# Kernel tuning notes

Measured on AMD Instinct MI355X. Metric: run time of the kernel, lower is better.

The kernel has to match this reference:

```python
import jax, jax.numpy as jnp
import numpy as np
import math

V, TB, C, H, L = 50257, 1024, 1024, 16, 8
B, T = 2, 1024
D = C // H


def setup_inputs() -> dict:
    key = jax.random.key(0)
    ks = jax.random.split(key, 16)
    s = 0.02
    n = lambda k, shp: (jax.random.normal(k, shp, jnp.float32) * s)
    inp = {
        "idx": jax.random.randint(ks[0], (B, T), 0, V),
        "tok_emb": n(ks[1], (V, C)),
        "pos_emb": n(ks[2], (1, TB, C)),
        # per-layer stacked params (torch Linear convention: W is [out, in])
        "Wq": n(ks[3], (L, C, C)), "bq": jnp.zeros((L, C)),
        "Wk": n(ks[4], (L, C, C)), "bk": jnp.zeros((L, C)),
        "Wv": n(ks[5], (L, C, C)), "bv": jnp.zeros((L, C)),
        "Wp": n(ks[6], (L, C, C)), "bp": jnp.zeros((L, C)),
        "ln1_w": jnp.ones((L, C)), "ln1_b": jnp.zeros((L, C)),
        "ln2_w": jnp.ones((L, C)), "ln2_b": jnp.zeros((L, C)),
        "W1": n(ks[7], (L, 4 * C, C)), "b1": jnp.zeros((L, 4 * C)),
        "W2": n(ks[8], (L, C, 4 * C)), "b2": jnp.zeros((L, C)),
        "lnf_w": jnp.ones((C,)), "lnf_b": jnp.zeros((C,)),
        "head_w": n(ks[9], (V, C)),
    }
    return inp


def _layer_norm(x, w, b, eps=1e-5):
    mu = x.mean(-1, keepdims=True)
    var = x.var(-1, keepdims=True)
    return (x - mu) * jax.lax.rsqrt(var + eps) * w + b


def _gpt_forward(idx, tok_emb, pos_emb, Wq, bq, Wk, bk, Wv, bv, Wp, bp,
                 ln1_w, ln1_b, ln2_w, ln2_b, W1, b1, W2, b2, lnf_w, lnf_b, head_w):
    b, t = idx.shape
    x = tok_emb[idx] + pos_emb[:, :t, :]  # [B, T, C]; drop = identity (eval)
    causal = jnp.tril(jnp.ones((t, t), dtype=bool))  # [T, T]
    scale = 1.0 / math.sqrt(D)

    def block(x, p):
        (wq, bq_, wk, bk_, wv, bv_, wp, bp_, l1w, l1b, l2w, l2b, w1, b1_, w2, b2_) = p
        h = _layer_norm(x, l1w, l1b)
        q = (h @ wq.T + bq_).reshape(b, t, H, D).transpose(0, 2, 1, 3)  # [B,H,T,D]
        k = (h @ wk.T + bk_).reshape(b, t, H, D).transpose(0, 2, 1, 3)
        v = (h @ wv.T + bv_).reshape(b, t, H, D).transpose(0, 2, 1, 3)
        att = jnp.einsum("bhqd,bhkd->bhqk", q, k) * scale
        att = jnp.where(causal, att, -jnp.inf)
        att = jax.nn.softmax(att, axis=-1)
        y = jnp.einsum("bhqk,bhkd->bhqd", att, v)
        y = y.transpose(0, 2, 1, 3).reshape(b, t, C)
        x = x + (y @ wp.T + bp_)
        h2 = _layer_norm(x, l2w, l2b)
        m = jax.nn.gelu(h2 @ w1.T + b1_, approximate=False)  # torch nn.GELU (erf)
        x = x + (m @ w2.T + b2_)
        return x, None

    params = (Wq, bq, Wk, bk, Wv, bv, Wp, bp, ln1_w, ln1_b, ln2_w, ln2_b, W1, b1, W2, b2)
    x, _ = jax.lax.scan(block, x, params)
    x = _layer_norm(x, lnf_w, lnf_b)
    logits = x @ head_w.T  # [B, T, V]
    return logits


def reference(idx, tok_emb, pos_emb, Wq, bq, Wk, bk, Wv, bv, Wp, bp,
              ln1_w, ln1_b, ln2_w, ln2_b, W1, b1, W2, b2, lnf_w, lnf_b, head_w):
    return _gpt_forward(idx, tok_emb, pos_emb, Wq, bq, Wk, bk, Wv, bv, Wp, bp,
                        ln1_w, ln1_b, ln2_w, ln2_b, W1, b1, W2, b2, lnf_w, lnf_b, head_w)
```

## Files before the change

### kernel.cpp

```cpp
#include <hip/hip_runtime.h>
#include <math.h>

#define V_ 50257
#define C_ 1024
#define H_ 16
#define L_ 8
#define B_ 2
#define T_ 1024
#define BT_ 2048
#define CC_ (C_*C_)
#define QLD_ 3072

typedef unsigned short ushort_t;
using bf16x8 = __attribute__((ext_vector_type(8))) short;
using f32x4  = __attribute__((ext_vector_type(4))) float;

__device__ __forceinline__ ushort_t f2bf(float f){
  union { float f; unsigned u; } a; a.f = f;
  unsigned r = a.u + 0x7fffu + ((a.u >> 16) & 1u);
  return (ushort_t)(r >> 16);
}

__device__ __forceinline__ float wave_sum(float v){
  #pragma unroll
  for(int o=32;o>0;o>>=1) v += __shfl_down(v,o,64);
  return v;
}

__global__ __launch_bounds__(256) void cvt_blk(const float* __restrict__ s, ushort_t* __restrict__ d,
    long inner4, int nblk, long dstStride4){
  long total = inner4 * nblk;
  for(long i = (long)blockIdx.x*256 + threadIdx.x; i < total; i += (long)gridDim.x*256){
    long blk = i / inner4, r = i - blk*inner4;
    float4 v = ((const float4*)s)[i];
    ushort4 o; o.x=f2bf(v.x); o.y=f2bf(v.y); o.z=f2bf(v.z); o.w=f2bf(v.w);
    ((ushort4*)d)[blk*dstStride4 + r] = o;
  }
}

__global__ __launch_bounds__(256) void pack_qkv_bias(const float* __restrict__ bq,
    const float* __restrict__ bk, const float* __restrict__ bv, float* __restrict__ dst){
  int i = blockIdx.x*256 + threadIdx.x;
  int l = i / QLD_, c = i - l*QLD_;
  float v;
  if(c < C_)            v = bq[l*C_ + c];
  else if(c < 2*C_)     v = bk[l*C_ + c - C_];
  else                  v = bv[l*C_ + c - 2*C_];
  dst[i] = v;
}

__global__ __launch_bounds__(256) void embed_kernel(const int* __restrict__ idx,
    const float* __restrict__ tok, const float* __restrict__ pos, float* __restrict__ x){
  int i = blockIdx.x*256 + threadIdx.x;
  int c = i & (C_-1); int bt = i >> 10; int t = bt & (T_-1);
  x[i] = tok[(size_t)idx[bt]*C_ + c] + pos[t*C_ + c];
}

__global__ __launch_bounds__(256) void ln_kernel(const float* in, const float* __restrict__ w,
    const float* __restrict__ b, float* outF, ushort_t* outB){
  int row = blockIdx.x;
  const float* xr = in + (size_t)row*C_;
  float vals[4]; float sum=0.f, sq=0.f;
  #pragma unroll
  for(int l=0;l<4;l++){ float v = xr[threadIdx.x + l*256]; vals[l]=v; sum+=v; sq+=v*v; }
  __shared__ float r1[4], r2[4];
  float s1 = wave_sum(sum), s2 = wave_sum(sq);
  int wid = threadIdx.x>>6, lane = threadIdx.x&63;
  if(lane==0){ r1[wid]=s1; r2[wid]=s2; }
  __syncthreads();
  float tot  = r1[0]+r1[1]+r1[2]+r1[3];
  float tot2 = r2[0]+r2[1]+r2[2]+r2[3];
  float mu  = tot * (1.f/C_);
  float var = tot2 * (1.f/C_) - mu*mu;
  float inv = rsqrtf(var + 1e-5f);
  #pragma unroll
  for(int l=0;l<4;l++){
    int c = threadIdx.x + l*256;
    float v = (vals[l]-mu)*inv*w[c] + b[c];
    if(outB) outB[(size_t)row*C_ + c] = f2bf(v);
    else     outF[(size_t)row*C_ + c] = v;
  }
}

template<int BN>
__global__ __launch_bounds__(256) void gemm_mfma(
    const ushort_t* __restrict__ A, const ushort_t* __restrict__ W,
    const float* __restrict__ bias, const float* resid,
    float* outF, ushort_t* outB,
    int M, int N, int K, int act, int nt)
{
  constexpr int BM = 128;
  constexpr int NSB = BN/16;
  constexpr int NBF = BN/32;
  __shared__ __align__(16) short sA[2][8*512];
  __shared__ __align__(16) short sB[2][NSB*512];
  const int tid  = threadIdx.x;
  const int lane = tid & 63, wid = tid >> 6;
  const int wr = wid >> 1, wc = wid & 1;
  const int nwg = gridDim.x * gridDim.y;
  const int lid = blockIdx.x + gridDim.x * blockIdx.y;
  const int swz = (lid & 7) * (nwg >> 3) + (lid >> 3);
  const int m0 = (swz % gridDim.x) * BM, n0 = (swz / gridDim.x) * BN;
  const int r16 = lane & 15, kq = lane >> 4;

  auto stage = [&](int buf, int k0){
    #pragma unroll
    for(int s2=0; s2<2; ++s2){
      int s = wid*2 + s2;
      const ushort_t* g = A + (size_t)(m0 + s*16 + r16)*K + k0 + kq*8;
      __builtin_amdgcn_global_load_lds((const __attribute__((address_space(1))) void*)g,
          (__attribute__((address_space(3))) void*)&sA[buf][s*512], 16, 0, 0);
    }
    #pragma unroll
    for(int s2=0; s2<NSB/4; ++s2){
      int s = wid*(NSB/4) + s2;
      int gn = n0 + s*16 + r16; if(gn >= N) gn = N-1;
      const ushort_t* g = W + (size_t)gn*K + k0 + kq*8;
      __builtin_amdgcn_global_load_lds((const __attribute__((address_space(1))) void*)g,
          (__attribute__((address_space(3))) void*)&sB[buf][s*512], 16, 0, 0);
    }
  };

  f32x4 acc[4][NBF];
  #pragma unroll
  for(int i=0;i<4;i++)
    #pragma unroll
    for(int j=0;j<NBF;j++) acc[i][j] = (f32x4){0.f,0.f,0.f,0.f};

  const int NT = K >> 5;
  stage(0, 0);
  int cur = 0;
  for(int t=0; t<NT; ++t){
    __syncthreads();
    if(t+1 < NT) stage(cur^1, (t+1)*32);
    bf16x8 af[4], bfr[NBF];
    #pragma unroll
    for(int m=0;m<4;m++) af[m] = *(const bf16x8*)&sA[cur][(wr*4+m)*512 + lane*8];
    #pragma unroll
    for(int n=0;n<NBF;n++) bfr[n] = *(const bf16x8*)&sB[cur][(wc*NBF+n)*512 + lane*8];
    #pragma unroll
    for(int m=0;m<4;m++)
      #pragma unroll
      for(int n=0;n<NBF;n++)
        acc[m][n] = __builtin_amdgcn_mfma_f32_16x16x32_bf16(af[m], bfr[n], acc[m][n], 0, 0, 0);
    cur ^= 1;
  }

  const int colb = n0 + wc*(BN/2);
  #pragma unroll
  for(int m=0;m<4;m++){
    int rowb = m0 + wr*64 + m*16 + kq*4;
    #pragma unroll
    for(int n=0;n<NBF;n++){
      int col = colb + n*16 + r16;
      if(col >= N) continue;
      float bv = bias ? bias[col] : 0.f;
      #pragma unroll
      for(int i=0;i<4;i++){
        int row = rowb + i;
        float v = acc[m][n][i] + bv;
        if(act) v = 0.5f*v*(1.f + erff(v*0.70710678118654752f));
        if(resid) v += resid[(size_t)row*N + col];
        if(outB) outB[(size_t)row*N + col] = f2bf(v);
        else if(nt) __builtin_nontemporal_store(v, &outF[(size_t)row*N + col]);
        else outF[(size_t)row*N + col] = v;
      }
    }
  }
}

__global__ __launch_bounds__(256) void flash_kernel(const ushort_t* __restrict__ qkv,
    ushort_t* __restrict__ y){
  const int tid = threadIdx.x, lane = tid & 63, wid = tid >> 6;
  const int r16 = lane & 15, kq = lane >> 4;
  const int lid = blockIdx.x + 16*blockIdx.y;
  const int swz = (lid & 7)*64 + (lid >> 3);
  const int qt = swz & 15, bh = swz >> 4;
  const int b = bh >> 4, h = bh & 15;
  const int q0 = qt*64, qw0 = q0 + wid*16;
  const int qa = qw0 + r16;

  __shared__ __align__(16) short Kt[8][512];
  __shared__ __align__(16) short VT[64][68];
  __shared__ __align__(16) short Pl[4][16][68];
  __shared__ __align__(16) short Ol[4][16][68];

  const size_t rowQ = (size_t)(b*T_ + qa)*QLD_ + h*64 + kq*8;
  bf16x8 qf0 = *(const bf16x8*)(qkv + rowQ);
  bf16x8 qf1 = *(const bf16x8*)(qkv + rowQ + 32);

  f32x4 acc[4];
  #pragma unroll
  for(int t=0;t<4;t++) acc[t] = (f32x4){0.f,0.f,0.f,0.f};
  float m_r = -INFINITY, l_r = 0.f;

  const int njt = qt + 1;
  for(int jt=0; jt<njt; ++jt){
    __syncthreads();
    #pragma unroll
    for(int s2=0;s2<2;s2++){
      int s = wid*2 + s2;
      const ushort_t* g = qkv + (size_t)(b*T_ + jt*64 + (s>>1)*16 + r16)*QLD_
                          + C_ + h*64 + (s&1)*32 + kq*8;
      __builtin_amdgcn_global_load_lds((const __attribute__((address_space(1))) void*)g,
          (__attribute__((address_space(3))) void*)&Kt[s][lane*8], 16, 0, 0);
    }
    #pragma unroll
    for(int a2=0;a2<2;a2++){
      int d0 = (a2*4 + wid)*8;
      bf16x8 vv = *(const bf16x8*)(qkv + (size_t)(b*T_ + jt*64 + lane)*QLD_ + 2*C_ + h*64 + d0);
      #pragma unroll
      for(int j=0;j<8;j++) VT[d0+j][lane] = vv[j];
    }
    __syncthreads();

    f32x4 st[4];
    __builtin_amdgcn_s_setprio(1);
    #pragma unroll
    for(int kr=0;kr<4;kr++){
      st[kr] = (f32x4){0.f,0.f,0.f,0.f};
      st[kr] = __builtin_amdgcn_mfma_f32_16x16x32_bf16(*(const bf16x8*)&Kt[kr*2+0][lane*8], qf0, st[kr], 0,0,0);
      st[kr] = __builtin_amdgcn_mfma_f32_16x16x32_bf16(*(const bf16x8*)&Kt[kr*2+1][lane*8], qf1, st[kr], 0,0,0);
    }
    __builtin_amdgcn_s_setprio(0);

    float vals[16]; float mx = m_r;
    if(jt == njt-1){
      #pragma unroll
      for(int kr=0;kr<4;kr++)
        #pragma unroll
        for(int i=0;i<4;i++){
          int ka = jt*64 + kr*16 + 4*kq + i;
          float v = (ka <= qa) ? st[kr][i]*0.125f : -INFINITY;
          vals[kr*4+i] = v; mx = fmaxf(mx, v);
        }
    } else {
      #pragma unroll
      for(int kr=0;kr<4;kr++)
        #pragma unroll
        for(int i=0;i<4;i++){
          float v = st[kr][i]*0.125f;
          vals[kr*4+i] = v; mx = fmaxf(mx, v);
        }
    }
    mx = fmaxf(mx, __shfl_xor(mx, 16, 64));
    mx = fmaxf(mx, __shfl_xor(mx, 32, 64));
    float alpha = __expf(m_r - mx);
    float ps = 0.f;
    #pragma unroll
    for(int kr=0;kr<4;kr++){
      float p0 = __expf(vals[kr*4+0]-mx), p1 = __expf(vals[kr*4+1]-mx);
      float p2 = __expf(vals[kr*4+2]-mx), p3 = __expf(vals[kr*4+3]-mx);
      ps += (p0+p1)+(p2+p3);
      unsigned u0 = (unsigned)f2bf(p0) | ((unsigned)f2bf(p1)<<16);
      unsigned u1 = (unsigned)f2bf(p2) | ((unsigned)f2bf(p3)<<16);
      *(unsigned*)&Pl[wid][r16][kr*16 + 4*kq]     = u0;
      *(unsigned*)&Pl[wid][r16][kr*16 + 4*kq + 2] = u1;
    }
    ps += __shfl_xor(ps, 16, 64);
    ps += __shfl_xor(ps, 32, 64);
    l_r = l_r*alpha + ps; m_r = mx;
    #pragma unroll
    for(int t=0;t<4;t++)
      #pragma unroll
      for(int j=0;j<4;j++) acc[t][j] *= alpha;

    union { bf16x8 v8; uint2 u2[2]; } pf, vf;
    __builtin_amdgcn_s_setprio(1);
    #pragma unroll
    for(int ks2=0; ks2<2; ks2++){
      pf.u2[0] = *(const uint2*)&Pl[wid][r16][ks2*32 + kq*8];
      pf.u2[1] = *(const uint2*)&Pl[wid][r16][ks2*32 + kq*8 + 4];
      #pragma unroll
      for(int db=0; db<4; db++){
        vf.u2[0] = *(const uint2*)&VT[16*db + r16][ks2*32 + kq*8];
        vf.u2[1] = *(const uint2*)&VT[16*db + r16][ks2*32 + kq*8 + 4];
        acc[db] = __builtin_amdgcn_mfma_f32_16x16x32_bf16(vf.v8, pf.v8, acc[db], 0,0,0);
      }
    }
    __builtin_amdgcn_s_setprio(0);
  }

  float linv = 1.f / l_r;
  #pragma unroll
  for(int db=0; db<4; db++)
    #pragma unroll
    for(int i=0;i<4;i++)
      Ol[wid][r16][16*db + 4*kq + i] = (short)f2bf(acc[db][i]*linv);
  int q = lane >> 2, c0 = (lane & 3)*16;
  const short* src = &Ol[wid][q][c0];
  uint2 a0 = *(const uint2*)(src+0), a1 = *(const uint2*)(src+4);
  uint2 a2 = *(const uint2*)(src+8), a3 = *(const uint2*)(src+12);
  ushort_t* dst = y + (size_t)(b*T_ + qw0 + q)*C_ + h*64 + c0;
  uint4 w0 = {a0.x, a0.y, a1.x, a1.y}, w1 = {a2.x, a2.y, a3.x, a3.y};
  *(uint4*)(dst+0) = w0;
  *(uint4*)(dst+8) = w1;
}

__global__ __launch_bounds__(256) void gemm_nt(const float* __restrict__ A, const float* __restrict__ W,
    const float* __restrict__ bias, const float* resid, float* Cm,
    int M, int N, int K, int act){
  __shared__ float As[16][68];
  __shared__ float Bs[16][68];
  int m0 = blockIdx.y*64, n0 = blockIdx.x*64;
  int tid = threadIdx.x;
  int tx = tid & 15, ty = tid >> 4;
  float acc[4][4] = {};
  for(int k0=0;k0<K;k0+=16){
    #pragma unroll
    for(int l=0;l<4;l++){
      int li = tid + l*256;
      int r = li >> 4, c = li & 15;
      int gm = m0 + r, gn = n0 + r, gk = k0 + c;
      As[c][r] = (gm<M) ? A[(size_t)gm*K + gk] : 0.f;
      Bs[c][r] = (gn<N) ? W[(size_t)gn*K + gk] : 0.f;
    }
    __syncthreads();
    #pragma unroll
    for(int k=0;k<16;k++){
      float4 av = *(const float4*)&As[k][ty*4];
      float4 bv = *(const float4*)&Bs[k][tx*4];
      float a[4] = {av.x, av.y, av.z, av.w};
      float b4[4] = {bv.x, bv.y, bv.z, bv.w};
      #pragma unroll
      for(int i=0;i<4;i++)
        #pragma unroll
        for(int j=0;j<4;j++)
          acc[i][j] = fmaf(a[i], b4[j], acc[i][j]);
    }
    __syncthreads();
  }
  #pragma unroll
  for(int i=0;i<4;i++){
    int m = m0 + ty*4 + i; if(m>=M) continue;
    #pragma unroll
    for(int j=0;j<4;j++){
      int n = n0 + tx*4 + j; if(n>=N) continue;
      float v = acc[i][j];
      if(bias) v += bias[n];
      if(act)  v = 0.5f*v*(1.f + erff(v*0.70710678118654752f));
      if(resid) v += resid[(size_t)m*N + n];
      Cm[(size_t)m*N + n] = v;
    }
  }
}

extern "C" void kernel_launch(void* const* d_in, const int* in_sizes, int n_in,
                              void* d_out, int out_size, void* d_ws, size_t ws_size,
                              hipStream_t stream) {
  const int*   idx  = (const int*)  d_in[0];
  const float* tok  = (const float*)d_in[1];
  const float* pos  = (const float*)d_in[2];
  const float* Wq   = (const float*)d_in[3];
  const float* bq   = (const float*)d_in[4];
  const float* Wk   = (const float*)d_in[5];
  const float* bk   = (const float*)d_in[6];
  const float* Wv   = (const float*)d_in[7];
  const float* bv   = (const float*)d_in[8];
  const float* Wp   = (const float*)d_in[9];
  const float* bp   = (const float*)d_in[10];
  const float* ln1w = (const float*)d_in[11];
  const float* ln1b = (const float*)d_in[12];
  const float* ln2w = (const float*)d_in[13];
  const float* ln2b = (const float*)d_in[14];
  const float* W1   = (const float*)d_in[15];
  const float* b1   = (const float*)d_in[16];
  const float* W2   = (const float*)d_in[17];
  const float* b2   = (const float*)d_in[18];
  const float* lnfw = (const float*)d_in[19];
  const float* lnfb = (const float*)d_in[20];
  const float* headw= (const float*)d_in[21];

  float* out = (float*)d_out;
  ushort_t* qkvb = (ushort_t*)(out);
  ushort_t* hb   = (ushort_t*)(out + 3145728);
  ushort_t* yb   = (ushort_t*)(out + 4194304);
  ushort_t* mb   = (ushort_t*)(out + 5242880);
  ushort_t* wqkv = (ushort_t*)(out + 9437184);
  ushort_t* wpb  = (ushort_t*)(out + 22020096);
  ushort_t* w1b  = (ushort_t*)(out + 26214400);
  ushort_t* w2b  = (ushort_t*)(out + 42991616);
  float*    bqkv = out + 59768832;
  float*    x    = (float*)d_ws;
  ushort_t* xb   = (ushort_t*)((float*)d_ws + 2097152);
  ushort_t* whb  = (ushort_t*)((float*)d_ws + 3145728);
  const bool big = ws_size >= (size_t)28877312 * 4;

  cvt_blk<<<2048,256,0,stream>>>(Wq, wqkv,          CC_/4, L_, 3*CC_/4);
  cvt_blk<<<2048,256,0,stream>>>(Wk, wqkv + CC_,    CC_/4, L_, 3*CC_/4);
  cvt_blk<<<2048,256,0,stream>>>(Wv, wqkv + 2*CC_,  CC_/4, L_, 3*CC_/4);
  cvt_blk<<<2048,256,0,stream>>>(Wp, wpb,  (long)L_*CC_/4,   1, (long)L_*CC_/4);
  cvt_blk<<<2048,256,0,stream>>>(W1, w1b,  (long)L_*CC_,     1, (long)L_*CC_);
  cvt_blk<<<2048,256,0,stream>>>(W2, w2b,  (long)L_*CC_,     1, (long)L_*CC_);
  if(big) cvt_blk<<<2048,256,0,stream>>>(headw, whb, (long)V_*C_/4, 1, (long)V_*C_/4);
  pack_qkv_bias<<<L_*QLD_/256,256,0,stream>>>(bq, bk, bv, bqkv);

  embed_kernel<<<BT_*C_/256, 256, 0, stream>>>(idx, tok, pos, x);

  for(int l=0;l<L_;l++){
    ln_kernel<<<BT_,256,0,stream>>>(x, ln1w + l*C_, ln1b + l*C_, nullptr, hb);
    gemm_mfma<128><<<dim3(BT_/128, QLD_/128),256,0,stream>>>(hb, wqkv + (size_t)l*3*CC_,
        bqkv + l*QLD_, nullptr, nullptr, qkvb, BT_, QLD_, C_, 0, 0);
    flash_kernel<<<dim3(T_/64, B_*H_),256,0,stream>>>(qkvb, yb);
    gemm_mfma<64><<<dim3(BT_/128, C_/64),256,0,stream>>>(yb, wpb + (size_t)l*CC_,
        bp + l*C_, x, x, nullptr, BT_, C_, C_, 0, 0);
    ln_kernel<<<BT_,256,0,stream>>>(x, ln2w + l*C_, ln2b + l*C_, nullptr, hb);
    gemm_mfma<128><<<dim3(BT_/128, 4*C_/128),256,0,stream>>>(hb, w1b + (size_t)l*4*CC_,
        b1 + (size_t)l*4*C_, nullptr, nullptr, mb, BT_, 4*C_, C_, 1, 0);
    gemm_mfma<64><<<dim3(BT_/128, C_/64),256,0,stream>>>(mb, w2b + (size_t)l*4*CC_,
        b2 + l*C_, x, x, nullptr, BT_, C_, 4*C_, 0, 0);
  }

  if(big){
    ln_kernel<<<BT_,256,0,stream>>>(x, lnfw, lnfb, nullptr, xb);
    gemm_mfma<128><<<dim3(BT_/128, (V_+127)/128),256,0,stream>>>(xb, whb,
        nullptr, nullptr, out, nullptr, BT_, V_, C_, 0, 1);
  } else {
    ln_kernel<<<BT_,256,0,stream>>>(x, lnfw, lnfb, x, nullptr);
    gemm_nt<<<dim3((V_+63)/64, BT_/64),256,0,stream>>>(x, headw, nullptr, nullptr, out,
                                                       BT_, V_, C_, 0);
  }
}
```

Measured before the change: 2.870 ms.

## Add 256x256 eight-wave pipelined GEMM for the LM head

Adds a new 512-thread GEMM kernel with 256x256 output tiles, K-steps of 64 and a four-phase schedule. In each phase it issues async global-to-LDS loads for a future half-tile while the waves run MFMAs on the current quadrant, gated by explicit vmcnt waits and raw barriers. It replaces the 128x128 gemm_mfma for the vocabulary projection, the largest GEMM, to raise data reuse and overlap loads with compute. In exchange it uses more LDS and registers, and the hand-placed waitcnt and barrier ordering is fragile. The remaining edits only introduce address-space macros.

```diff
diff --git a/kernel.cpp b/kernel.cpp
--- a/kernel.cpp
+++ b/kernel.cpp
@@ -14,6 +14,12 @@
 typedef unsigned short ushort_t;
 using bf16x8 = __attribute__((ext_vector_type(8))) short;
 using f32x4  = __attribute__((ext_vector_type(4))) float;
+
+#define AS1 __attribute__((address_space(1)))
+#define AS3 __attribute__((address_space(3)))
+#define VMCNT6() asm volatile("s_waitcnt vmcnt(6)" ::: "memory")
+#define VMCNT0() asm volatile("s_waitcnt vmcnt(0)" ::: "memory")
+#define RBAR()   asm volatile("s_barrier" ::: "memory")
 
 __device__ __forceinline__ ushort_t f2bf(float f){
   union { float f; unsigned u; } a; a.f = f;
@@ -108,16 +114,16 @@
     for(int s2=0; s2<2; ++s2){
       int s = wid*2 + s2;
       const ushort_t* g = A + (size_t)(m0 + s*16 + r16)*K + k0 + kq*8;
-      __builtin_amdgcn_global_load_lds((const __attribute__((address_space(1))) void*)g,
-          (__attribute__((address_space(3))) void*)&sA[buf][s*512], 16, 0, 0);
+      __builtin_amdgcn_global_load_lds((const AS1 void*)g,
+          (AS3 void*)&sA[buf][s*512], 16, 0, 0);
     }
     #pragma unroll
     for(int s2=0; s2<NSB/4; ++s2){
       int s = wid*(NSB/4) + s2;
       int gn = n0 + s*16 + r16; if(gn >= N) gn = N-1;
       const ushort_t* g = W + (size_t)gn*K + k0 + kq*8;
-      __builtin_amdgcn_global_load_lds((const __attribute__((address_space(1))) void*)g,
-          (__attribute__((address_space(3))) void*)&sB[buf][s*512], 16, 0, 0);
+      __builtin_amdgcn_global_load_lds((const AS1 void*)g,
+          (AS3 void*)&sB[buf][s*512], 16, 0, 0);
     }
   };
 
@@ -167,6 +173,151 @@
       }
     }
   }
+}
+
+__global__ __launch_bounds__(512) void gemm_8ph(
+    const ushort_t* __restrict__ A, const ushort_t* __restrict__ W,
+    float* __restrict__ outF, int M, int N, int K, int gx)
+{
+  __shared__ __align__(16) short sA[2][2][8192];
+  __shared__ __align__(16) short sB[2][2][8192];
+  const int tid = threadIdx.x, lane = tid & 63;
+  const int wid = tid >> 6, wm = wid & 1, wn = wid >> 1;
+  const int r16 = lane & 15, kq = lane >> 4;
+  const int nwg = gridDim.x;
+  const int L = blockIdx.x;
+  const int swz = (L & 7) * (nwg >> 3) + (L >> 3);
+  const int m0 = (swz % gx) * 256, n0 = (swz / gx) * 256;
+
+  auto stage = [&](int buf, int half, int isB, int k0){
+    const ushort_t* base = isB ? W : A;
+    const int off0 = (isB ? n0 : m0) + half*128;
+    short* dst0 = isB ? &sB[buf][half][0] : &sA[buf][half][0];
+    #pragma unroll
+    for(int i=0;i<2;i++){
+      int sub = i*4 + (tid>>7);
+      int rem = tid & 127;
+      int row = off0 + sub*16 + (rem & 15);
+      if(isB && row >= N) row = N-1;
+      int kk = k0 + ((rem>>6)&1)*32 + ((rem>>4)&3)*8;
+      __builtin_amdgcn_global_load_lds((const AS1 void*)(base + (size_t)row*K + kk),
+          (AS3 void*)(dst0 + i*4096 + tid*8), 16, 0, 0);
+    }
+  };
+
+  f32x4 acc[2][2][4][2];
+  #pragma unroll
+  for(int a=0;a<2;a++)
+    #pragma unroll
+    for(int b=0;b<2;b++)
+      #pragma unroll
+      for(int m=0;m<4;m++)
+        #pragma unroll
+        for(int n=0;n<2;n++) acc[a][b][m][n] = (f32x4){0.f,0.f,0.f,0.f};
+
+  const int NT = K >> 6;
+  stage(0,0,0, 0); stage(0,0,1, 0); stage(0,1,1, 0); stage(0,1,0, 0);
+  if(NT>1){ stage(1,0,0, 64); stage(1,0,1, 64); stage(1,1,1, 64); }
+  VMCNT6();
+  RBAR();
+
+  bf16x8 af[4][2], bfr[2][2][2];
+
+  for(int t=0; t<NT; ++t){
+    const int buf = t & 1;
+    const int k1 = (t+1)<<6, k2 = (t+2)<<6;
+    const bool s1 = (t+1) < NT, s2 = (t+2) < NT;
+
+    if(s1) stage(buf^1, 1, 0, k1);
+    #pragma unroll
+    for(int m=0;m<4;m++)
+      #pragma unroll
+      for(int ks=0;ks<2;ks++)
+        af[m][ks] = *(const bf16x8*)&sA[buf][0][(wm*4+m)*1024 + ks*512 + lane*8];
+    #pragma unroll
+    for(int n=0;n<2;n++)
+      #pragma unroll
+      for(int ks=0;ks<2;ks++)
+        bfr[0][n][ks] = *(const bf16x8*)&sB[buf][0][(wn*2+n)*1024 + ks*512 + lane*8];
+    RBAR();
+    __builtin_amdgcn_s_setprio(1);
+    #pragma unroll
+    for(int m=0;m<4;m++)
+      #pragma unroll
+      for(int n=0;n<2;n++)
+        #pragma unroll
+        for(int ks=0;ks<2;ks++)
+          acc[0][0][m][n] = __builtin_amdgcn_mfma_f32_16x16x32_bf16(af[m][ks], bfr[0][n][ks], acc[0][0][m][n], 0,0,0);
+    __builtin_amdgcn_s_setprio(0);
+    RBAR();
+
+    if(s2) stage(buf, 0, 0, k2);
+    #pragma unroll
+    for(int n=0;n<2;n++)
+      #pragma unroll
+      for(int ks=0;ks<2;ks++)
+        bfr[1][n][ks] = *(const bf16x8*)&sB[buf][1][(wn*2+n)*1024 + ks*512 + lane*8];
+    RBAR();
+    __builtin_amdgcn_s_setprio(1);
+    #pragma unroll
+    for(int m=0;m<4;m++)
+      #pragma unroll
+      for(int n=0;n<2;n++)
+        #pragma unroll
+        for(int ks=0;ks<2;ks++)
+          acc[0][1][m][n] = __builtin_amdgcn_mfma_f32_16x16x32_bf16(af[m][ks], bfr[1][n][ks], acc[0][1][m][n], 0,0,0);
+    __builtin_amdgcn_s_setprio(0);
+    RBAR();
+
+    if(s2) stage(buf, 0, 1, k2);
+    #pragma unroll
+    for(int m=0;m<4;m++)
+      #pragma unroll
+      for(int ks=0;ks<2;ks++)
+        af[m][ks] = *(const bf16x8*)&sA[buf][1][(wm*4+m)*1024 + ks*512 + lane*8];
+    RBAR();
+    __builtin_amdgcn_s_setprio(1);
+    #pragma unroll
+    for(int m=0;m<4;m++)
+      #pragma unroll
+      for(int n=0;n<2;n++)
+        #pragma unroll
+        for(int ks=0;ks<2;ks++)
+          acc[1][1][m][n] = __builtin_amdgcn_mfma_f32_16x16x32_bf16(af[m][ks], bfr[1][n][ks], acc[1][1][m][n], 0,0,0);
+    __builtin_amdgcn_s_setprio(0);
+    RBAR();
+
+    if(s2) stage(buf, 1, 1, k2);
+    if(s2) { VMCNT6(); } else { VMCNT0(); }
+    RBAR();
+    __builtin_amdgcn_s_setprio(1);
+    #pragma unroll
+    for(int m=0;m<4;m++)
+      #pragma unroll
+      for(int n=0;n<2;n++)
+        #pragma unroll
+        for(int ks=0;ks<2;ks++)
+          acc[1][0][m][n] = __builtin_amdgcn_mfma_f32_16x16x32_bf16(af[m][ks], bfr[0][n][ks], acc[1][0][m][n], 0,0,0);
+    __builtin_amdgcn_s_setprio(0);
+    RBAR();
+  }
+
+  #pragma unroll
+  for(int mh=0;mh<2;mh++)
+    #pragma unroll
+    for(int nh=0;nh<2;nh++)
+      #pragma unroll
+      for(int m=0;m<4;m++){
+        int rowb = m0 + mh*128 + wm*64 + m*16 + kq*4;
+        #pragma unroll
+        for(int n=0;n<2;n++){
+          int col = n0 + nh*128 + wn*32 + n*16 + r16;
+          if(col >= N) continue;
+          #pragma unroll
+          for(int i=0;i<4;i++)
+            __builtin_nontemporal_store(acc[mh][nh][m][n][i], &outF[(size_t)(rowb+i)*N + col]);
+        }
+      }
 }
 
 __global__ __launch_bounds__(256) void flash_kernel(const ushort_t* __restrict__ qkv,
@@ -202,8 +353,8 @@
       int s = wid*2 + s2;
       const ushort_t* g = qkv + (size_t)(b*T_ + jt*64 + (s>>1)*16 + r16)*QLD_
                           + C_ + h*64 + (s&1)*32 + kq*8;
-      __builtin_amdgcn_global_load_lds((const __attribute__((address_space(1))) void*)g,
-          (__attribute__((address_space(3))) void*)&Kt[s][lane*8], 16, 0, 0);
+      __builtin_amdgcn_global_load_lds((const AS1 void*)g,
+          (AS3 void*)&Kt[s][lane*8], 16, 0, 0);
     }
     #pragma unroll
     for(int a2=0;a2<2;a2++){
@@ -413,8 +564,8 @@
 
   if(big){
     ln_kernel<<<BT_,256,0,stream>>>(x, lnfw, lnfb, nullptr, xb);
-    gemm_mfma<128><<<dim3(BT_/128, (V_+127)/128),256,0,stream>>>(xb, whb,
-        nullptr, nullptr, out, nullptr, BT_, V_, C_, 0, 1);
+    gemm_8ph<<<dim3((BT_/256) * ((V_+255)/256)),512,0,stream>>>(xb, whb, out,
+        BT_, V_, C_, BT_/256);
   } else {
     ln_kernel<<<BT_,256,0,stream>>>(x, lnfw, lnfb, x, nullptr);
     gemm_nt<<<dim3((V_+63)/64, BT_/64),256,0,stream>>>(x, headw, nullptr, nullptr, out,
```

Result: no change. 2.867 ms (-0.1%).

## Double-buffer K and V tiles in flash attention to overlap loads with compute

Applied to the files above, without the earlier changes.

The flash attention kernel now keeps two LDS buffers for K and transposed V. The next tile's K (async global-to-LDS) and V (into registers) are prefetched while the current tile's QK and PV MFMAs run, then V is written to the alternate buffer at the end of the iteration. This cuts the loop to one barrier per tile and hides global load latency, at the cost of doubled LDS for K/V, extra live registers, and possible lower occupancy. The GEMM change is a macro cleanup only.

```diff
diff --git a/kernel.cpp b/kernel.cpp
--- a/kernel.cpp
+++ b/kernel.cpp
@@ -14,6 +14,10 @@
 typedef unsigned short ushort_t;
 using bf16x8 = __attribute__((ext_vector_type(8))) short;
 using f32x4  = __attribute__((ext_vector_type(4))) float;
+
+#define AS1 __attribute__((address_space(1)))
+#define AS3 __attribute__((address_space(3)))
+#define VMCNT0() asm volatile("s_waitcnt vmcnt(0)" ::: "memory")
 
 __device__ __forceinline__ ushort_t f2bf(float f){
   union { float f; unsigned u; } a; a.f = f;
@@ -108,16 +112,16 @@
     for(int s2=0; s2<2; ++s2){
       int s = wid*2 + s2;
       const ushort_t* g = A + (size_t)(m0 + s*16 + r16)*K + k0 + kq*8;
-      __builtin_amdgcn_global_load_lds((const __attribute__((address_space(1))) void*)g,
-          (__attribute__((address_space(3))) void*)&sA[buf][s*512], 16, 0, 0);
+      __builtin_amdgcn_global_load_lds((const AS1 void*)g,
+          (AS3 void*)&sA[buf][s*512], 16, 0, 0);
     }
     #pragma unroll
     for(int s2=0; s2<NSB/4; ++s2){
       int s = wid*(NSB/4) + s2;
       int gn = n0 + s*16 + r16; if(gn >= N) gn = N-1;
       const ushort_t* g = W + (size_t)gn*K + k0 + kq*8;
-      __builtin_amdgcn_global_load_lds((const __attribute__((address_space(1))) void*)g,
-          (__attribute__((address_space(3))) void*)&sB[buf][s*512], 16, 0, 0);
+      __builtin_amdgcn_global_load_lds((const AS1 void*)g,
+          (AS3 void*)&sB[buf][s*512], 16, 0, 0);
     }
   };
 
@@ -180,8 +184,8 @@
   const int q0 = qt*64, qw0 = q0 + wid*16;
   const int qa = qw0 + r16;
 
-  __shared__ __align__(16) short Kt[8][512];
-  __shared__ __align__(16) short VT[64][68];
+  __shared__ __align__(16) short Kt[2][8][512];
+  __shared__ __align__(16) short VT[2][64][68];
   __shared__ __align__(16) short Pl[4][16][68];
   __shared__ __align__(16) short Ol[4][16][68];
 
@@ -189,38 +193,52 @@
   bf16x8 qf0 = *(const bf16x8*)(qkv + rowQ);
   bf16x8 qf1 = *(const bf16x8*)(qkv + rowQ + 32);
 
-  f32x4 acc[4];
-  #pragma unroll
-  for(int t=0;t<4;t++) acc[t] = (f32x4){0.f,0.f,0.f,0.f};
-  float m_r = -INFINITY, l_r = 0.f;
-
-  const int njt = qt + 1;
-  for(int jt=0; jt<njt; ++jt){
-    __syncthreads();
+  auto stageK = [&](int buf, int jt){
     #pragma unroll
     for(int s2=0;s2<2;s2++){
       int s = wid*2 + s2;
       const ushort_t* g = qkv + (size_t)(b*T_ + jt*64 + (s>>1)*16 + r16)*QLD_
                           + C_ + h*64 + (s&1)*32 + kq*8;
-      __builtin_amdgcn_global_load_lds((const __attribute__((address_space(1))) void*)g,
-          (__attribute__((address_space(3))) void*)&Kt[s][lane*8], 16, 0, 0);
-    }
-    #pragma unroll
-    for(int a2=0;a2<2;a2++){
-      int d0 = (a2*4 + wid)*8;
-      bf16x8 vv = *(const bf16x8*)(qkv + (size_t)(b*T_ + jt*64 + lane)*QLD_ + 2*C_ + h*64 + d0);
-      #pragma unroll
-      for(int j=0;j<8;j++) VT[d0+j][lane] = vv[j];
-    }
+      __builtin_amdgcn_global_load_lds((const AS1 void*)g,
+          (AS3 void*)&Kt[buf][s][lane*8], 16, 0, 0);
+    }
+  };
+
+  f32x4 acc[4];
+  #pragma unroll
+  for(int t=0;t<4;t++) acc[t] = (f32x4){0.f,0.f,0.f,0.f};
+  float m_r = -INFINITY, l_r = 0.f;
+
+  {
+    stageK(0, 0);
+    const ushort_t* vg = qkv + (size_t)(b*T_ + lane)*QLD_ + 2*C_ + h*64;
+    bf16x8 va = *(const bf16x8*)(vg + wid*8);
+    bf16x8 vb = *(const bf16x8*)(vg + 32 + wid*8);
+    VMCNT0();
+    #pragma unroll
+    for(int j=0;j<8;j++){ VT[0][wid*8+j][lane]=va[j]; VT[0][32+wid*8+j][lane]=vb[j]; }
     __syncthreads();
+  }
+
+  const int njt = qt + 1;
+  for(int jt=0; jt<njt; ++jt){
+    const int cur = jt & 1;
+    const bool more = (jt+1) < njt;
+    bf16x8 vr0, vr1;
+    if(more){
+      stageK(cur^1, jt+1);
+      const ushort_t* vg = qkv + (size_t)(b*T_ + (jt+1)*64 + lane)*QLD_ + 2*C_ + h*64;
+      vr0 = *(const bf16x8*)(vg + wid*8);
+      vr1 = *(const bf16x8*)(vg + 32 + wid*8);
+    }
 
     f32x4 st[4];
     __builtin_amdgcn_s_setprio(1);
     #pragma unroll
     for(int kr=0;kr<4;kr++){
       st[kr] = (f32x4){0.f,0.f,0.f,0.f};
-      st[kr] = __builtin_amdgcn_mfma_f32_16x16x32_bf16(*(const bf16x8*)&Kt[kr*2+0][lane*8], qf0, st[kr], 0,0,0);
-      st[kr] = __builtin_amdgcn_mfma_f32_16x16x32_bf16(*(const bf16x8*)&Kt[kr*2+1][lane*8], qf1, st[kr], 0,0,0);
+      st[kr] = __builtin_amdgcn_mfma_f32_16x16x32_bf16(*(const bf16x8*)&Kt[cur][kr*2+0][lane*8], qf0, st[kr], 0,0,0);
+      st[kr] = __builtin_amdgcn_mfma_f32_16x16x32_bf16(*(const bf16x8*)&Kt[cur][kr*2+1][lane*8], qf1, st[kr], 0,0,0);
     }
     __builtin_amdgcn_s_setprio(0);
 
@@ -273,12 +291,19 @@
       pf.u2[1] = *(const uint2*)&Pl[wid][r16][ks2*32 + kq*8 + 4];
       #pragma unroll
       for(int db=0; db<4; db++){
-        vf.u2[0] = *(const uint2*)&VT[16*db + r16][ks2*32 + kq*8];
-        vf.u2[1] = *(const uint2*)&VT[16*db + r16][ks2*32 + kq*8 + 4];
+        vf.u2[0] = *(const uint2*)&VT[cur][16*db + r16][ks2*32 + kq*8];
+        vf.u2[1] = *(const uint2*)&VT[cur][16*db + r16][ks2*32 + kq*8 + 4];
         acc[db] = __builtin_amdgcn_mfma_f32_16x16x32_bf16(vf.v8, pf.v8, acc[db], 0,0,0);
       }
     }
     __builtin_amdgcn_s_setprio(0);
+
+    if(more){
+      VMCNT0();
+      #pragma unroll
+      for(int j=0;j<8;j++){ VT[cur^1][wid*8+j][lane]=vr0[j]; VT[cur^1][32+wid*8+j][lane]=vr1[j]; }
+    }
+    __syncthreads();
   }
 
   float linv = 1.f / l_r;
```

Result: no change. 2.871 ms (+0.0%).
